# Optimization experiments

Measured on AMD Instinct MI355X. Metric: run time of the kernel, lower is better.

## Reference

```python
import jax, jax.numpy as jnp
import numpy as np

L = 2        # num stacked decoder layers (len(layer_indexes))
S = 2048     # seq_len (prefill)
H = 2048     # hidden_size
NH = 16      # num_heads == num_key_value_heads
D = 128      # head_dim
I = 5632     # intermediate_size
EPS = 1e-6   # rms_norm_eps
NEG = -1e9   # additive causal mask value


def setup_inputs() -> dict:
    key = jax.random.key(0)
    ks = jax.random.split(key, 10)
    scale = 0.02
    hidden_states = jax.random.normal(ks[0], (1, S, H), jnp.float32)
    # causal additive mask, matching the attention_mask parameter in prefill mode
    attention_mask = jnp.where(jnp.tril(jnp.ones((S, S), bool)), 0.0, NEG)[None, None].astype(jnp.float32)
    position_ids = jnp.arange(S, dtype=jnp.int32)[None]
    # Llama rotary tables: (max_seq, head_dim), cos/sin repeated over both halves
    inv_freq = 1.0 / (10000.0 ** (jnp.arange(0, D, 2, dtype=jnp.float32) / D))
    ang = jnp.arange(S, dtype=jnp.float32)[:, None] * inv_freq[None, :]   # [S, D/2]
    cached_cos = jnp.concatenate([jnp.cos(ang), jnp.cos(ang)], axis=-1)   # [S, D]
    cached_sin = jnp.concatenate([jnp.sin(ang), jnp.sin(ang)], axis=-1)
    wq = jax.random.normal(ks[1], (L, H, H), jnp.float32) * scale
    wk = jax.random.normal(ks[2], (L, H, H), jnp.float32) * scale
    wv = jax.random.normal(ks[3], (L, H, H), jnp.float32) * scale
    wo = jax.random.normal(ks[4], (L, H, H), jnp.float32) * scale
    w_gate = jax.random.normal(ks[5], (L, I, H), jnp.float32) * scale
    w_up = jax.random.normal(ks[6], (L, I, H), jnp.float32) * scale
    w_down = jax.random.normal(ks[7], (L, H, I), jnp.float32) * scale
    ln1 = jnp.ones((L, H), jnp.float32)
    ln2 = jnp.ones((L, H), jnp.float32)
    return {"hidden_states": hidden_states, "attention_mask": attention_mask,
            "cached_cos": cached_cos, "cached_sin": cached_sin,
            "wq": wq, "wk": wk, "wv": wv, "wo": wo,
            "w_gate": w_gate, "w_up": w_up, "w_down": w_down,
            "ln1": ln1, "ln2": ln2, "position_ids": position_ids}


def _rms_norm(x, w):
    # variance = mean(x^2) (no mean subtraction), then scale -- exactly as in build_decoder
    var = jnp.mean(x * x, axis=-1, keepdims=True)
    return (x / jnp.sqrt(var + EPS)) * w


def _rotate_half(x):
    x1, x2 = jnp.split(x, 2, axis=-1)
    return jnp.concatenate([-x2, x1], axis=-1)


def _rope(x, cos, sin):
    return x * cos + _rotate_half(x) * sin


def _forward(hidden_states, attention_mask, cached_cos, cached_sin,
             wq, wk, wv, wo, w_gate, w_up, w_down, ln1, ln2, position_ids):
    pos = position_ids[0]                              # [S]
    cos = cached_cos[pos][None, None]                  # [1,1,S,D]
    sin = cached_sin[pos][None, None]
    inv_sqrt_d = 1.0 / np.sqrt(D).astype(np.float32)
    x = hidden_states                                  # [1,S,H]
    for i in range(L):
        h = _rms_norm(x, ln1[i])
        q = (h @ wq[i].T).reshape(1, S, NH, D).transpose(0, 2, 1, 3)  # [1,NH,S,D]
        k = (h @ wk[i].T).reshape(1, S, NH, D).transpose(0, 2, 1, 3)
        v = (h @ wv[i].T).reshape(1, S, NH, D).transpose(0, 2, 1, 3)
        q = _rope(q, cos, sin)
        k = _rope(k, cos, sin)
        scores = jnp.einsum('bhqd,bhkd->bhqk', q, k) * inv_sqrt_d + attention_mask
        attn = jax.nn.softmax(scores, axis=-1)
        o = jnp.einsum('bhqk,bhkd->bhqd', attn, v)
        o = o.transpose(0, 2, 1, 3).reshape(1, S, H)
        x = x + o @ wo[i].T
        h = _rms_norm(x, ln2[i])
        mlp = (jax.nn.silu(h @ w_gate[i].T) * (h @ w_up[i].T)) @ w_down[i].T
        x = x + mlp
    return x


def reference(hidden_states, attention_mask, cached_cos, cached_sin,
              wq, wk, wv, wo, w_gate, w_up, w_down, ln1, ln2, position_ids):
    return _forward(hidden_states, attention_mask, cached_cos, cached_sin,
                    wq, wk, wv, wo, w_gate, w_up, w_down, ln1, ln2, position_ids)
```

## Files before the change

kernel.cpp:

```cpp
#include <hip/hip_runtime.h>
#include <hip/hip_bf16.h>

constexpr int kL = 2;
constexpr int kS = 2048;
constexpr int kH = 2048;
constexpr int kNH = 16;
constexpr int kD = 128;
constexpr int kI = 5632;

using s16x8 = __attribute__((ext_vector_type(8))) short;
using s16x4 = __attribute__((ext_vector_type(4))) short;
using f32x4 = __attribute__((ext_vector_type(4))) float;

__device__ __forceinline__ float b2f(short s) {
  union { unsigned u; float f; } v;
  v.u = ((unsigned)(unsigned short)s) << 16;
  return v.f;
}
__device__ __forceinline__ short f2bs(float f) {
  __hip_bfloat16 h = __float2bfloat16(f);
  union { __hip_bfloat16 h; short s; } u;
  u.h = h;
  return u.s;
}

__device__ __forceinline__ void lds16(const void* g, void* l) {
  __builtin_amdgcn_global_load_lds(
      (const __attribute__((address_space(1))) void*)g,
      (__attribute__((address_space(3))) void*)l, 16, 0, 0);
}

__device__ __forceinline__ void swz_block(int gx, int& bx, int& by) {
  const int gy = gridDim.y;
  const int lin = by * gx + bx;
  if ((gx & 3) == 0 && (gy & 1) == 0) {
    const int cx = gx >> 2, cy = gy >> 1;
    const int xcd = lin & 7;
    const int s = lin >> 3;
    bx = (xcd & 3) * cx + s / cy;
    by = (xcd >> 2) * cy + s % cy;
  } else if (((gx * gy) & 7) == 0) {
    const int cpx = (gx * gy) >> 3;
    const int l2 = (lin & 7) * cpx + (lin >> 3);
    bx = l2 % gx;
    by = l2 / gx;
  }
}

__global__ __launch_bounds__(256) void cvt_all(const float* __restrict__ q,
                                               const float* __restrict__ k,
                                               const float* __restrict__ v,
                                               const float* __restrict__ o,
                                               const float* __restrict__ g,
                                               const float* __restrict__ u,
                                               const float* __restrict__ d,
                                               short* __restrict__ dst) {
  constexpr int HH8 = (kH * kH) / 8;
  constexpr int IH8 = (kI * kH) / 8;
  constexpr int tot = 4 * HH8 + 3 * IH8;
  for (int i = blockIdx.x * blockDim.x + threadIdx.x; i < tot; i += gridDim.x * blockDim.x) {
    const float* src;
    int off;
    if (i < 4 * HH8) {
      const int s = i >> 19;
      off = i & (HH8 - 1);
      src = s == 0 ? q : s == 1 ? k : s == 2 ? v : o;
    } else {
      const int j = i - 4 * HH8;
      if (j < 2 * IH8) {
        const int r = j >> 8;
        const int c8 = j & 255;
        src = (r & 1) ? u : g;
        off = (r >> 1) * 256 + c8;
      } else {
        src = d;
        off = j - 2 * IH8;
      }
    }
    const float4 a = ((const float4*)src)[2 * off];
    const float4 b = ((const float4*)src)[2 * off + 1];
    s16x8 ov;
    ov[0] = f2bs(a.x); ov[1] = f2bs(a.y); ov[2] = f2bs(a.z); ov[3] = f2bs(a.w);
    ov[4] = f2bs(b.x); ov[5] = f2bs(b.y); ov[6] = f2bs(b.z); ov[7] = f2bs(b.w);
    ((s16x8*)dst)[i] = ov;
  }
}

template <int EPI>
__global__ __launch_bounds__(256) void gemm_db(const short* __restrict__ A,
                                               const short* __restrict__ B,
                                               short* __restrict__ C0,
                                               short* __restrict__ C1,
                                               short* __restrict__ C2,
                                               float* __restrict__ Cf,
                                               int M, int N, int K) {
  __shared__ short As0[128 * 64], Bs0[128 * 64];
  __shared__ short As1[128 * 64], Bs1[128 * 64];
  const int t = threadIdx.x;
  const int lane = t & 63, wid = t >> 6;
  int bx = blockIdx.x, by = blockIdx.y;
  swz_block(gridDim.x, bx, by);
  const int m0 = by * 128, n0 = bx * 128;
  const int Ksub = K / (int)gridDim.z;
  const int kbase = blockIdx.z * Ksub;
  const int wr = (wid >> 1) * 64, wc = (wid & 1) * 64;
  const int fr = lane & 15, g4 = lane >> 4;

  const int srow = (lane >> 3);
  const int scol = (((lane & 7) << 4) ^ (srow << 4)) >> 1;

  f32x4 acc[4][4] = {};

  auto stage = [&](short* Ad, short* Bd, int k0) {
    #pragma unroll
    for (int c = 0; c < 4; ++c) {
      const int chunk = wid * 4 + c;
      const int e0 = chunk * 512;
      const int row = chunk * 8 + srow;
      lds16(A + (size_t)(m0 + row) * K + kbase + k0 + scol, Ad + e0);
      lds16(B + (size_t)(n0 + row) * K + kbase + k0 + scol, Bd + e0);
    }
  };

  auto compute = [&](const short* Xs, const short* Ys) {
    #pragma unroll
    for (int ks = 0; ks < 2; ++ks) {
      s16x8 a[4], b[4];
      #pragma unroll
      for (int m = 0; m < 4; ++m) {
        const int r = wr + m * 16 + fr;
        a[m] = *(const s16x8*)&Xs[r * 64 + (((ks * 4 + g4) ^ (r & 7)) << 3)];
      }
      #pragma unroll
      for (int n = 0; n < 4; ++n) {
        const int r = wc + n * 16 + fr;
        b[n] = *(const s16x8*)&Ys[r * 64 + (((ks * 4 + g4) ^ (r & 7)) << 3)];
      }
      #pragma unroll
      for (int m = 0; m < 4; ++m)
        #pragma unroll
        for (int n = 0; n < 4; ++n)
          acc[m][n] = __builtin_amdgcn_mfma_f32_16x16x32_bf16(a[m], b[n], acc[m][n], 0, 0, 0);
    }
  };

  const int nt = Ksub >> 6;
  stage(As0, Bs0, 0);
  __syncthreads();
  for (int tt = 0; tt < nt; tt += 2) {
    stage(As1, Bs1, (tt + 1) << 6);
    compute(As0, Bs0);
    __syncthreads();
    if (tt + 2 < nt) stage(As0, Bs0, (tt + 2) << 6);
    compute(As1, Bs1);
    __syncthreads();
  }

  #pragma unroll
  for (int m = 0; m < 4; ++m) {
    #pragma unroll
    for (int n = 0; n < 4; ++n) {
      const int rb = m0 + wr + m * 16 + g4 * 4;
      const int col = n0 + wc + n * 16 + fr;
      if (EPI == 1) {
        #pragma unroll
        for (int j = 0; j < 4; ++j)
          Cf[(size_t)(rb + j) * N + col] += acc[m][n][j];
      } else if (EPI == 6) {
        #pragma unroll
        for (int j = 0; j < 4; ++j)
          unsafeAtomicAdd(&Cf[(size_t)(rb + j) * N + col], acc[m][n][j]);
      } else if (EPI == 3) {
        const int seg = n0 >> 11;
        const int cl = col - (seg << 11);
        if (seg == 0) {
          #pragma unroll
          for (int j = 0; j < 4; ++j) C0[(size_t)(rb + j) * 2048 + cl] = f2bs(acc[m][n][j]);
        } else if (seg == 1) {
          #pragma unroll
          for (int j = 0; j < 4; ++j) C1[(size_t)(rb + j) * 2048 + cl] = f2bs(acc[m][n][j]);
        } else {
          s16x4 pk;
          #pragma unroll
          for (int j = 0; j < 4; ++j) pk[j] = f2bs(acc[m][n][j]);
          *(s16x4*)&C2[(size_t)cl * M + rb] = pk;
        }
      } else {
        #pragma unroll
        for (int j = 0; j < 4; ++j) {
          const float gv = acc[m][n][j];
          const float pv = __shfl_xor(gv, 1);
          if ((fr & 1) == 0) {
            const float s = gv / (1.f + __expf(-gv));
            C0[(size_t)(rb + j) * kI + (col >> 1)] = f2bs(s * pv);
          }
        }
      }
    }
  }
}

template <int EPI>
__global__ __launch_bounds__(256) void gemm_btf(const short* __restrict__ A,
                                                const float* __restrict__ B,
                                                short* __restrict__ Cb,
                                                float* __restrict__ Cf,
                                                int M, int N, int K) {
  __shared__ short As[128 * 32];
  __shared__ short Bs[128 * 32];
  const int t = threadIdx.x;
  const int lane = t & 63, wid = t >> 6;
  int bx = blockIdx.x, by = blockIdx.y;
  swz_block(gridDim.x, bx, by);
  const int m0 = by * 128, n0 = bx * 128;
  const int wr = (wid >> 1) * 64, wc = (wid & 1) * 64;
  const int fr = lane & 15, h8 = (lane >> 4) * 8;
  const int brow = t >> 1, bcol = (t & 1) * 16;
  const float* bsrc = B + (size_t)(n0 + brow) * K + bcol;

  f32x4 acc[4][4] = {};

  for (int k0 = 0; k0 < K; k0 += 32) {
    const float4 bv0 = *(const float4*)(bsrc + k0);
    const float4 bv1 = *(const float4*)(bsrc + k0 + 4);
    const float4 bv2 = *(const float4*)(bsrc + k0 + 8);
    const float4 bv3 = *(const float4*)(bsrc + k0 + 12);
    __syncthreads();
    {
      const float bf[16] = {bv0.x, bv0.y, bv0.z, bv0.w, bv1.x, bv1.y, bv1.z, bv1.w,
                            bv2.x, bv2.y, bv2.z, bv2.w, bv3.x, bv3.y, bv3.z, bv3.w};
      s16x8 wlo, whi;
      #pragma unroll
      for (int j = 0; j < 8; ++j) { wlo[j] = f2bs(bf[j]); whi[j] = f2bs(bf[8 + j]); }
      *(s16x8*)&Bs[brow * 32 + bcol] = wlo;
      *(s16x8*)&Bs[brow * 32 + bcol + 8] = whi;
    }
    #pragma unroll
    for (int c = 0; c < 2; ++c) {
      const int e0 = c * 2048 + wid * 512;
      const int e = e0 + lane * 8;
      const int row = e >> 5, col = e & 31;
      lds16(A + (size_t)(m0 + row) * K + k0 + col, (void*)(As + e0));
    }
    __syncthreads();

    s16x8 a[4], b[4];
    #pragma unroll
    for (int m = 0; m < 4; ++m) a[m] = *(const s16x8*)&As[(wr + m * 16 + fr) * 32 + h8];
    #pragma unroll
    for (int n = 0; n < 4; ++n) b[n] = *(const s16x8*)&Bs[(wc + n * 16 + fr) * 32 + h8];
    #pragma unroll
    for (int m = 0; m < 4; ++m)
      #pragma unroll
      for (int n = 0; n < 4; ++n)
        acc[m][n] = __builtin_amdgcn_mfma_f32_16x16x32_bf16(a[m], b[n], acc[m][n], 0, 0, 0);
  }

  const int g4 = lane >> 4;
  #pragma unroll
  for (int m = 0; m < 4; ++m) {
    #pragma unroll
    for (int n = 0; n < 4; ++n) {
      const int rb = m0 + wr + m * 16 + g4 * 4;
      const int col = n0 + wc + n * 16 + fr;
      if (EPI == 0) {
        #pragma unroll
        for (int j = 0; j < 4; ++j)
          Cb[(size_t)(rb + j) * N + col] = f2bs(acc[m][n][j]);
      } else if (EPI == 1) {
        #pragma unroll
        for (int j = 0; j < 4; ++j)
          Cf[(size_t)(rb + j) * N + col] += acc[m][n][j];
      } else {
        s16x4 pk;
        #pragma unroll
        for (int j = 0; j < 4; ++j) pk[j] = f2bs(acc[m][n][j]);
        *(s16x4*)&Cb[(size_t)col * M + rb] = pk;
      }
    }
  }
}

__global__ __launch_bounds__(256) void rmsnorm_k(const float* __restrict__ x,
                                                 const float* __restrict__ w,
                                                 short* __restrict__ h) {
  const int row = blockIdx.x, t = threadIdx.x;
  const float4* xr = (const float4*)(x + (size_t)row * kH);
  const float4 v0 = xr[2 * t], v1 = xr[2 * t + 1];
  float ss = v0.x * v0.x + v0.y * v0.y + v0.z * v0.z + v0.w * v0.w +
             v1.x * v1.x + v1.y * v1.y + v1.z * v1.z + v1.w * v1.w;
  #pragma unroll
  for (int off = 1; off < 64; off <<= 1) ss += __shfl_xor(ss, off);
  __shared__ float red[4];
  if ((t & 63) == 0) red[t >> 6] = ss;
  __syncthreads();
  ss = red[0] + red[1] + red[2] + red[3];
  const float rs = rsqrtf(ss * (1.0f / kH) + 1e-6f);
  const float4 w0 = ((const float4*)w)[2 * t];
  const float4 w1 = ((const float4*)w)[2 * t + 1];
  const float xv[8] = {v0.x, v0.y, v0.z, v0.w, v1.x, v1.y, v1.z, v1.w};
  const float wv[8] = {w0.x, w0.y, w0.z, w0.w, w1.x, w1.y, w1.z, w1.w};
  s16x8 o;
  #pragma unroll
  for (int j = 0; j < 8; ++j) o[j] = f2bs(xv[j] * rs * wv[j]);
  *(s16x8*)&h[(size_t)row * kH + t * 8] = o;
}

__global__ __launch_bounds__(256) void rope_k(short* __restrict__ q, short* __restrict__ k,
                                              const float* __restrict__ cosb,
                                              const float* __restrict__ sinb,
                                              const int* __restrict__ pos) {
  const int s = blockIdx.x;
  const int p = pos[s];
  const size_t rowb = (size_t)s * kH;
  for (int idx = threadIdx.x; idx < kNH * 64; idx += 256) {
    const int hh = idx >> 6, d = idx & 63;
    const float c = cosb[p * kD + d];
    const float sn = sinb[p * kD + d];
    const size_t i1 = rowb + hh * kD + d, i2 = i1 + 64;
    const float q1 = b2f(q[i1]), q2 = b2f(q[i2]);
    q[i1] = f2bs(q1 * c - q2 * sn);
    q[i2] = f2bs(q2 * c + q1 * sn);
    const float k1 = b2f(k[i1]), k2 = b2f(k[i2]);
    k[i1] = f2bs(k1 * c - k2 * sn);
    k[i2] = f2bs(k2 * c + k1 * sn);
  }
}

__global__ __launch_bounds__(256) void attn_k(const short* __restrict__ q,
                                              const short* __restrict__ k,
                                              const short* __restrict__ vt,
                                              short* __restrict__ o) {
  __shared__ short Kl[2][64 * 128];
  __shared__ short Vl[2][128 * 64];
  __shared__ short Pl[4][16 * 72];
  const int h = blockIdx.x;
  const int y = blockIdx.y;
  const int qi = (y < 16) ? y : 47 - y;
  const int t = threadIdx.x;
  const int lane = t & 63, wid = t >> 6;
  const int fr = lane & 15, g4 = lane >> 4;
  const int q0 = qi * 64 + wid * 16;

  s16x8 aq[4];
  {
    const short* qp = q + (size_t)(q0 + fr) * kH + h * kD;
    #pragma unroll
    for (int ks = 0; ks < 4; ++ks) aq[ks] = *(const s16x8*)(qp + ks * 32 + g4 * 8);
  }
  f32x4 acco[8] = {};
  float mrun[4], lrun[4];
  #pragma unroll
  for (int j = 0; j < 4; ++j) { mrun[j] = -3.0e30f; lrun[j] = 0.f; }

  s16x8 kreg[4], vreg[4];
  auto loadt = [&](int tt) {
    const int kv0 = tt * 64;
    #pragma unroll
    for (int c = 0; c < 4; ++c) {
      const int b = c * 4096 + t * 16;
      kreg[c] = *(const s16x8*)(k + (size_t)(kv0 + (b >> 8)) * kH + h * kD + ((b & 255) >> 1));
      vreg[c] = *(const s16x8*)(vt + (size_t)(h * kD + (b >> 7)) * kS + kv0 + ((b & 127) >> 1));
    }
  };
  auto writet = [&](int buf) {
    #pragma unroll
    for (int c = 0; c < 4; ++c) {
      const int b = c * 4096 + t * 16;
      const int kr = b >> 8, kc = b & 255;
      *(s16x8*)((char*)Kl[buf] + kr * 256 + (kc ^ ((kr & 7) << 4))) = kreg[c];
      const int vr = b >> 7, vc = b & 127;
      *(s16x8*)((char*)Vl[buf] + vr * 128 + (vc ^ ((vr & 7) << 4))) = vreg[c];
    }
  };

  loadt(0);
  writet(0);
  __syncthreads();

  for (int tt = 0; tt <= qi; ++tt) {
    const int kv0 = tt * 64;
    const int cur = tt & 1;
    if (tt < qi) loadt(tt + 1);

    f32x4 sc[4] = {};
    __builtin_amdgcn_s_setprio(1);
    #pragma unroll
    for (int ks = 0; ks < 4; ++ks) {
      const int ch16 = ks * 4 + g4;
      #pragma unroll
      for (int nf = 0; nf < 4; ++nf) {
        const int row = nf * 16 + fr;
        const s16x8 bk =
            *(const s16x8*)((const char*)Kl[cur] + row * 256 + ((ch16 ^ (row & 7)) << 4));
        sc[nf] = __builtin_amdgcn_mfma_f32_16x16x32_bf16(aq[ks], bk, sc[nf], 0, 0, 0);
      }
    }
    __builtin_amdgcn_s_setprio(0);

    float val[4][4];
    #pragma unroll
    for (int nf = 0; nf < 4; ++nf) {
      #pragma unroll
      for (int j = 0; j < 4; ++j) {
        float v = sc[nf][j] * 0.08838834764831845f;
        if (tt == qi) {
          const int colg = kv0 + nf * 16 + fr;
          const int rowg = q0 + g4 * 4 + j;
          if (colg > rowg) v -= 1.0e9f;
        }
        val[nf][j] = v;
      }
    }

    #pragma unroll
    for (int j = 0; j < 4; ++j) {
      float rm = fmaxf(fmaxf(val[0][j], val[1][j]), fmaxf(val[2][j], val[3][j]));
      rm = fmaxf(rm, __shfl_xor(rm, 1));
      rm = fmaxf(rm, __shfl_xor(rm, 2));
      rm = fmaxf(rm, __shfl_xor(rm, 4));
      rm = fmaxf(rm, __shfl_xor(rm, 8));
      const float mnew = fmaxf(mrun[j], rm);
      const float corr = __expf(mrun[j] - mnew);
      mrun[j] = mnew;
      float ps = 0.f;
      #pragma unroll
      for (int nf = 0; nf < 4; ++nf) {
        const float p = __expf(val[nf][j] - mnew);
        ps += p;
        Pl[wid][(g4 * 4 + j) * 72 + nf * 16 + fr] = f2bs(p);
      }
      ps += __shfl_xor(ps, 1);
      ps += __shfl_xor(ps, 2);
      ps += __shfl_xor(ps, 4);
      ps += __shfl_xor(ps, 8);
      lrun[j] = lrun[j] * corr + ps;
      #pragma unroll
      for (int nf = 0; nf < 8; ++nf) acco[nf][j] *= corr;
    }

    __builtin_amdgcn_s_setprio(1);
    #pragma unroll
    for (int ks = 0; ks < 2; ++ks) {
      const s16x8 ap = *(const s16x8*)(&Pl[wid][fr * 72 + ks * 32 + g4 * 8]);
      const int ch16 = ks * 4 + g4;
      #pragma unroll
      for (int nf = 0; nf < 8; ++nf) {
        const int dd = nf * 16 + fr;
        const s16x8 bv =
            *(const s16x8*)((const char*)Vl[cur] + dd * 128 + ((ch16 ^ (dd & 7)) << 4));
        acco[nf] = __builtin_amdgcn_mfma_f32_16x16x32_bf16(ap, bv, acco[nf], 0, 0, 0);
      }
    }
    __builtin_amdgcn_s_setprio(0);

    if (tt < qi) writet(cur ^ 1);
    __syncthreads();
  }

  #pragma unroll
  for (int nf = 0; nf < 8; ++nf) {
    #pragma unroll
    for (int j = 0; j < 4; ++j) {
      const int rowg = q0 + g4 * 4 + j;
      o[(size_t)rowg * kH + h * kD + nf * 16 + fr] = f2bs(acco[nf][j] / lrun[j]);
    }
  }
}

__global__ void silu_mul(short* __restrict__ g, const short* __restrict__ u, int n8) {
  for (int i = blockIdx.x * blockDim.x + threadIdx.x; i < n8; i += gridDim.x * blockDim.x) {
    const s16x8 gv = ((const s16x8*)g)[i];
    const s16x8 uv = ((const s16x8*)u)[i];
    s16x8 o;
    #pragma unroll
    for (int j = 0; j < 8; ++j) {
      const float gf = b2f(gv[j]);
      const float s = gf / (1.f + __expf(-gf));
      o[j] = f2bs(s * b2f(uv[j]));
    }
    ((s16x8*)g)[i] = o;
  }
}

extern "C" void kernel_launch(void* const* d_in, const int* in_sizes, int n_in,
                              void* d_out, int out_size, void* d_ws, size_t ws_size,
                              hipStream_t stream) {
  (void)in_sizes; (void)n_in; (void)out_size;
  const float* hidden = (const float*)d_in[0];
  const float* cosb = (const float*)d_in[2];
  const float* sinb = (const float*)d_in[3];
  const float* wq = (const float*)d_in[4];
  const float* wk = (const float*)d_in[5];
  const float* wv = (const float*)d_in[6];
  const float* wo = (const float*)d_in[7];
  const float* wg = (const float*)d_in[8];
  const float* wu = (const float*)d_in[9];
  const float* wd = (const float*)d_in[10];
  const float* ln1 = (const float*)d_in[11];
  const float* ln2 = (const float*)d_in[12];
  const int* pos = (const int*)d_in[13];
  float* out = (float*)d_out;

  char* p = (char*)d_ws;
  float* x  = (float*)p;  p += (size_t)kS * kH * 4;
  short* hb = (short*)p;  p += (size_t)kS * kH * 2;
  char* U = p;            p += (size_t)kS * kI * 4;
  short* qb = (short*)(U);
  short* kb = (short*)(U + (size_t)kS * kH * 2);
  short* vtb = (short*)(U + (size_t)kS * kH * 4);
  short* ob = (short*)(U + (size_t)kS * kH * 6);
  short* gb = (short*)(U);
  short* ub = (short*)(U + (size_t)kS * kI * 2);
  short* wbuf = (short*)p;
  const size_t nHH = (size_t)kH * kH, nIH = (size_t)kI * kH;
  const size_t need = (size_t)(p - (char*)d_ws) + (4 * nHH + 3 * nIH) * 2;
  const bool pre = ws_size >= need;

  short* wqb = wbuf;
  short* wob = wqb + 3 * nHH;
  short* wgu = wob + nHH;
  short* wdb = wgu + 2 * nIH;

  hipMemcpyAsync(x, hidden, (size_t)kS * kH * 4, hipMemcpyDeviceToDevice, stream);
  for (int l = 0; l < kL; ++l) {
    rmsnorm_k<<<kS, 256, 0, stream>>>(x, ln1 + (size_t)l * kH, hb);
    if (pre) {
      cvt_all<<<2048, 256, 0, stream>>>(wq + l * nHH, wk + l * nHH, wv + l * nHH,
                                        wo + l * nHH, wg + l * nIH, wu + l * nIH,
                                        wd + l * nIH, wbuf);
      gemm_db<3><<<dim3(6144 / 128, kS / 128), 256, 0, stream>>>(
          hb, wqb, qb, kb, vtb, nullptr, kS, 6144, kH);
      rope_k<<<kS, 256, 0, stream>>>(qb, kb, cosb, sinb, pos);
      attn_k<<<dim3(kNH, kS / 64), 256, 0, stream>>>(qb, kb, vtb, ob);
      gemm_db<6><<<dim3(kH / 128, kS / 128, 2), 256, 0, stream>>>(
          ob, wob, nullptr, nullptr, nullptr, x, kS, kH, kH);
      rmsnorm_k<<<kS, 256, 0, stream>>>(x, ln2 + (size_t)l * kH, hb);
      gemm_db<5><<<dim3(11264 / 128, kS / 128), 256, 0, stream>>>(
          hb, wgu, gb, nullptr, nullptr, nullptr, kS, 11264, kH);
      gemm_db<6><<<dim3(kH / 128, kS / 128, 2), 256, 0, stream>>>(
          gb, wdb, nullptr, nullptr, nullptr, x, kS, kH, kI);
    } else {
      gemm_btf<0><<<dim3(kH / 128, kS / 128), 256, 0, stream>>>(hb, wq + l * nHH, qb, nullptr, kS, kH, kH);
      gemm_btf<0><<<dim3(kH / 128, kS / 128), 256, 0, stream>>>(hb, wk + l * nHH, kb, nullptr, kS, kH, kH);
      gemm_btf<2><<<dim3(kH / 128, kS / 128), 256, 0, stream>>>(hb, wv + l * nHH, vtb, nullptr, kS, kH, kH);
      rope_k<<<kS, 256, 0, stream>>>(qb, kb, cosb, sinb, pos);
      attn_k<<<dim3(kNH, kS / 64), 256, 0, stream>>>(qb, kb, vtb, ob);
      gemm_btf<1><<<dim3(kH / 128, kS / 128), 256, 0, stream>>>(ob, wo + l * nHH, nullptr, x, kS, kH, kH);
      rmsnorm_k<<<kS, 256, 0, stream>>>(x, ln2 + (size_t)l * kH, hb);
      gemm_btf<0><<<dim3(kI / 128, kS / 128), 256, 0, stream>>>(hb, wg + l * nIH, gb, nullptr, kS, kI, kH);
      gemm_btf<0><<<dim3(kI / 128, kS / 128), 256, 0, stream>>>(hb, wu + l * nIH, ub, nullptr, kS, kI, kH);
      silu_mul<<<1408, 256, 0, stream>>>(gb, ub, kS * kI / 8);
      gemm_btf<1><<<dim3(kH / 128, kS / 128), 256, 0, stream>>>(gb, wd + l * nIH, nullptr, x, kS, kH, kI);
    }
  }
  hipMemcpyAsync(out, x, (size_t)kS * kH * 4, hipMemcpyDeviceToDevice, stream);
}
```

Baseline: 905.0 us.

## Read K/V tiles directly from global memory in attention, dropping LDS staging

The attention kernel no longer stages K and V tiles into double-buffered shared memory with swizzling. Each wave now loads its MFMA B-operands directly from global memory, relying on the L1/L2 caches for reuse across the four waves. This removes the LDS writes and per-tile block barriers and frees LDS, which could raise occupancy. The cost is four times the global or cache traffic for K/V and no explicit prefetch to hide load latency.

```diff
diff --git a/kernel.cpp b/kernel.cpp
--- a/kernel.cpp
+++ b/kernel.cpp
@@ -331,8 +331,6 @@
                                               const short* __restrict__ k,
                                               const short* __restrict__ vt,
                                               short* __restrict__ o) {
-  __shared__ short Kl[2][64 * 128];
-  __shared__ short Vl[2][128 * 64];
   __shared__ short Pl[4][16 * 72];
   const int h = blockIdx.x;
   const int y = blockIdx.y;
@@ -348,51 +346,26 @@
     #pragma unroll
     for (int ks = 0; ks < 4; ++ks) aq[ks] = *(const s16x8*)(qp + ks * 32 + g4 * 8);
   }
+  const short* kp = k + h * kD;
+  const short* vp = vt + (size_t)h * kD * kS;
+
   f32x4 acco[8] = {};
   float mrun[4], lrun[4];
   #pragma unroll
   for (int j = 0; j < 4; ++j) { mrun[j] = -3.0e30f; lrun[j] = 0.f; }
 
-  s16x8 kreg[4], vreg[4];
-  auto loadt = [&](int tt) {
-    const int kv0 = tt * 64;
-    #pragma unroll
-    for (int c = 0; c < 4; ++c) {
-      const int b = c * 4096 + t * 16;
-      kreg[c] = *(const s16x8*)(k + (size_t)(kv0 + (b >> 8)) * kH + h * kD + ((b & 255) >> 1));
-      vreg[c] = *(const s16x8*)(vt + (size_t)(h * kD + (b >> 7)) * kS + kv0 + ((b & 127) >> 1));
-    }
-  };
-  auto writet = [&](int buf) {
-    #pragma unroll
-    for (int c = 0; c < 4; ++c) {
-      const int b = c * 4096 + t * 16;
-      const int kr = b >> 8, kc = b & 255;
-      *(s16x8*)((char*)Kl[buf] + kr * 256 + (kc ^ ((kr & 7) << 4))) = kreg[c];
-      const int vr = b >> 7, vc = b & 127;
-      *(s16x8*)((char*)Vl[buf] + vr * 128 + (vc ^ ((vr & 7) << 4))) = vreg[c];
-    }
-  };
-
-  loadt(0);
-  writet(0);
-  __syncthreads();
-
   for (int tt = 0; tt <= qi; ++tt) {
     const int kv0 = tt * 64;
-    const int cur = tt & 1;
-    if (tt < qi) loadt(tt + 1);
 
     f32x4 sc[4] = {};
     __builtin_amdgcn_s_setprio(1);
     #pragma unroll
     for (int ks = 0; ks < 4; ++ks) {
-      const int ch16 = ks * 4 + g4;
+      const int co = (ks * 4 + g4) * 8;
       #pragma unroll
       for (int nf = 0; nf < 4; ++nf) {
-        const int row = nf * 16 + fr;
-        const s16x8 bk =
-            *(const s16x8*)((const char*)Kl[cur] + row * 256 + ((ch16 ^ (row & 7)) << 4));
+        const int row = kv0 + nf * 16 + fr;
+        const s16x8 bk = *(const s16x8*)(kp + (size_t)row * kH + co);
         sc[nf] = __builtin_amdgcn_mfma_f32_16x16x32_bf16(aq[ks], bk, sc[nf], 0, 0, 0);
       }
     }
@@ -443,19 +416,15 @@
     #pragma unroll
     for (int ks = 0; ks < 2; ++ks) {
       const s16x8 ap = *(const s16x8*)(&Pl[wid][fr * 72 + ks * 32 + g4 * 8]);
-      const int ch16 = ks * 4 + g4;
+      const int co = (ks * 4 + g4) * 8;
       #pragma unroll
       for (int nf = 0; nf < 8; ++nf) {
         const int dd = nf * 16 + fr;
-        const s16x8 bv =
-            *(const s16x8*)((const char*)Vl[cur] + dd * 128 + ((ch16 ^ (dd & 7)) << 4));
+        const s16x8 bv = *(const s16x8*)(vp + (size_t)dd * kS + kv0 + co);
         acco[nf] = __builtin_amdgcn_mfma_f32_16x16x32_bf16(ap, bv, acco[nf], 0, 0, 0);
       }
     }
     __builtin_amdgcn_s_setprio(0);
-
-    if (tt < qi) writet(cur ^ 1);
-    __syncthreads();
   }
 
   #pragma unroll
```

After: 1.052 ms. +16.2%, slower.
